# Performance work log

Hardware: AMD Instinct MI355X
Metric: run time of the kernel (lower is better)

Reference implementation:

```python
import jax, jax.numpy as jnp
import numpy as np

TEXT_VOCAB = 32000
CB = 1024          # audio_codebook_size
NCB = 8            # audio_num_codebooks
H = 2048           # hidden_size
NH = 16            # attention heads
NKV = 4            # kv heads (GQA)
HD = H // NH       # head dim = 128
FF = 8192          # ffn intermediate
L = 2              # num layers
EPS = 1e-5


def rmsnorm(x, w):
    v = jnp.mean(x * x, axis=-1, keepdims=True)
    return x * jax.lax.rsqrt(v + EPS) * w


def rope(x, pos):
    # x: [B,S,h,d], rotate-half style RoPE
    d = x.shape[-1]
    inv = 1.0 / (10000.0 ** (jnp.arange(0, d, 2, dtype=jnp.float32) / d))
    ang = pos[:, None] * inv[None, :]                 # [S, d/2]
    cos = jnp.cos(ang)[None, :, None, :]
    sin = jnp.sin(ang)[None, :, None, :]
    x1, x2 = x[..., : d // 2], x[..., d // 2 :]
    return jnp.concatenate([x1 * cos - x2 * sin, x2 * cos + x1 * sin], axis=-1)


def attention(x, wq, wk, wv, wo, pos, mask_bias):
    B, S, _ = x.shape
    q = (x @ wq).reshape(B, S, NH, HD)
    k = (x @ wk).reshape(B, S, NKV, HD)
    v = (x @ wv).reshape(B, S, NKV, HD)
    q = rope(q, pos)
    k = rope(k, pos)
    k = jnp.repeat(k, NH // NKV, axis=2)
    v = jnp.repeat(v, NH // NKV, axis=2)
    scores = jnp.einsum('bqhd,bkhd->bhqk', q, k) / np.float32(np.sqrt(HD))
    p = jax.nn.softmax(scores + mask_bias, axis=-1)
    o = jnp.einsum('bhqk,bkhd->bqhd', p, v).reshape(B, S, NH * HD)
    return o @ wo


def mlp(x, wfc, wproj):
    return jax.nn.silu(x @ wfc) @ wproj


def setup_inputs() -> dict:
    key = jax.random.key(0)
    ks = jax.random.split(key, 20)
    s = 0.02
    inp = {
        'input_ids': jax.random.randint(ks[0], (1, 2048), 0, TEXT_VOCAB + CB, dtype=jnp.int64 if jax.config.jax_enable_x64 else jnp.int32),
        'vocab_emb': jax.random.normal(ks[1], (TEXT_VOCAB, H), jnp.float32) * s,
        'audio_emb': jax.random.normal(ks[2], (NCB * CB, H), jnp.float32) * s,
        'ln_in_text': jnp.ones((L, H), jnp.float32),
        'ln_in_audio': jnp.ones((L, H), jnp.float32),
        'ln_post_text': jnp.ones((L, H), jnp.float32),
        'ln_post_audio': jnp.ones((L, H), jnp.float32),
        'wq': jax.random.normal(ks[3], (L, H, NH * HD), jnp.float32) * s,
        'wk': jax.random.normal(ks[4], (L, H, NKV * HD), jnp.float32) * s,
        'wv': jax.random.normal(ks[5], (L, H, NKV * HD), jnp.float32) * s,
        'wo': jax.random.normal(ks[6], (L, NH * HD, H), jnp.float32) * s,
        'wfc_text': jax.random.normal(ks[7], (L, H, FF), jnp.float32) * s,
        'wproj_text': jax.random.normal(ks[8], (L, FF, H), jnp.float32) * s,
        'wfc_audio': jax.random.normal(ks[9], (L, H, FF), jnp.float32) * s,
        'wproj_audio': jax.random.normal(ks[10], (L, FF, H), jnp.float32) * s,
        'ln_f': jnp.ones((H,), jnp.float32),
    }
    return inp


def reference(input_ids, vocab_emb, audio_emb, ln_in_text, ln_in_audio,
              ln_post_text, ln_post_audio, wq, wk, wv, wo,
              wfc_text, wproj_text, wfc_audio, wproj_audio, ln_f):
    B, S = input_ids.shape
    amask = input_ids > TEXT_VOCAB - 1                      # [B,S] audio-token mask
    text_tok = jnp.where(amask, TEXT_VOCAB - 1, input_ids)
    text_e = vocab_emb[text_tok]                            # [B,S,H]
    audio_tok = jnp.where(amask, input_ids - TEXT_VOCAB, 0)
    shift = (jnp.arange(NCB) * CB)[:, None, None]           # [NCB,1,1]
    audio_e = audio_emb[audio_tok[None] + shift].sum(0)     # sum over codebooks -> [B,S,H]
    h = jnp.where(amask[..., None], audio_e, text_e)

    pos = jnp.arange(S, dtype=jnp.float32)
    causal = jnp.tril(jnp.ones((S, S), bool))
    mask_bias = jnp.where(causal, 0.0, -1e9).astype(jnp.float32)[None, None]
    m = amask[..., None]

    for i in range(L):
        res = h
        hn = jnp.where(m, rmsnorm(h, ln_in_audio[i]), rmsnorm(h, ln_in_text[i]))
        h = res + attention(hn, wq[i], wk[i], wv[i], wo[i], pos, mask_bias)
        res = h
        t = mlp(rmsnorm(h, ln_post_text[i]), wfc_text[i], wproj_text[i])
        a = mlp(rmsnorm(h, ln_post_audio[i]), wfc_audio[i], wproj_audio[i])
        h = res + jnp.where(m, a, t)

    return rmsnorm(h, ln_f)
```

## Files before the change

### kernel.cpp

```cpp
#include <hip/hip_runtime.h>
#include <hip/hip_bf16.h>
#include <math.h>

#define S_LEN 2048
#define HID   2048

typedef __bf16 bf16x8 __attribute__((ext_vector_type(8)));
typedef float  f32x4  __attribute__((ext_vector_type(4)));

__device__ __forceinline__ unsigned short f2b(float x) {
  __hip_bfloat16 h = __float2bfloat16(x);
  return __builtin_bit_cast(unsigned short, h);
}

__device__ __forceinline__ float block_sum_256(float v) {
  __shared__ float red[4];
  #pragma unroll
  for (int o = 32; o > 0; o >>= 1) v += __shfl_down(v, o, 64);
  if ((threadIdx.x & 63) == 0) red[threadIdx.x >> 6] = v;
  __syncthreads();
  v = red[0] + red[1] + red[2] + red[3];
  __syncthreads();
  return v;
}

__device__ __forceinline__ float block_max_256(float v) {
  __shared__ float redm[4];
  #pragma unroll
  for (int o = 32; o > 0; o >>= 1) v = fmaxf(v, __shfl_down(v, o, 64));
  if ((threadIdx.x & 63) == 0) redm[threadIdx.x >> 6] = v;
  __syncthreads();
  v = fmaxf(fmaxf(redm[0], redm[1]), fmaxf(redm[2], redm[3]));
  __syncthreads();
  return v;
}

__global__ __launch_bounds__(256) void embed_kernel(
    const int* __restrict__ ids, const float* __restrict__ vemb,
    const float* __restrict__ aemb, float* __restrict__ h, int* __restrict__ amask) {
  const int s = blockIdx.x;
  const int id = ids[s];
  const bool am = id > 31999;
  if (threadIdx.x == 0) amask[s] = am ? 1 : 0;
  const int d0 = threadIdx.x * 8;
  float out[8];
  if (am) {
    const int at = id - 32000;
    #pragma unroll
    for (int u = 0; u < 8; u++) out[u] = 0.f;
    for (int cb = 0; cb < 8; cb++) {
      const float* src = aemb + (long)(at + cb * 1024) * HID + d0;
      #pragma unroll
      for (int u = 0; u < 8; u++) out[u] += src[u];
    }
  } else {
    const float* src = vemb + (long)id * HID + d0;
    #pragma unroll
    for (int u = 0; u < 8; u++) out[u] = src[u];
  }
  float* dst = h + (long)s * HID + d0;
  #pragma unroll
  for (int u = 0; u < 8; u++) dst[u] = out[u];
}

__global__ __launch_bounds__(256) void partition_rows(
    const int* __restrict__ ids, int* __restrict__ apos, int* __restrict__ cnt) {
  __shared__ int ca[256];
  __shared__ int sc[257];
  const int t = threadIdx.x;
  int m[8], loc = 0;
  #pragma unroll
  for (int i = 0; i < 8; i++) { m[i] = ids[t * 8 + i] > 31999 ? 1 : 0; loc += m[i]; }
  ca[t] = loc;
  __syncthreads();
  if (t == 0) {
    int run = 0;
    for (int i = 0; i < 256; i++) { sc[i] = run; run += ca[i]; }
    sc[256] = run;
  }
  __syncthreads();
  int off = sc[t];
  #pragma unroll
  for (int i = 0; i < 8; i++) {
    const int s = t * 8 + i;
    if (m[i]) { apos[s] = off; off++; }
    else apos[s] = -1;
  }
  if (t == 0) { cnt[0] = sc[256]; cnt[1] = (sc[256] + 127) & ~127; }
}

__global__ __launch_bounds__(256) void transposew(
    const float* __restrict__ W, int ldw, unsigned short* __restrict__ Wt, int K, int N) {
  __shared__ float t[64][65];
  const int k0 = blockIdx.y * 64, n0 = blockIdx.x * 64;
  const int q = threadIdx.x & 15;
  const int r0 = threadIdx.x >> 4;
  #pragma unroll
  for (int i = 0; i < 4; i++) {
    const int row = r0 + i * 16;
    const float4 v = *(const float4*)(W + (long)(k0 + row) * ldw + n0 + q * 4);
    t[row][q * 4 + 0] = v.x; t[row][q * 4 + 1] = v.y;
    t[row][q * 4 + 2] = v.z; t[row][q * 4 + 3] = v.w;
  }
  __syncthreads();
  #pragma unroll
  for (int i = 0; i < 4; i++) {
    const int n = r0 + i * 16;
    ushort4 o;
    o.x = f2b(t[q * 4 + 0][n]); o.y = f2b(t[q * 4 + 1][n]);
    o.z = f2b(t[q * 4 + 2][n]); o.w = f2b(t[q * 4 + 3][n]);
    *(ushort4*)(Wt + (long)(n0 + n) * K + k0 + q * 4) = o;
  }
}

__global__ __launch_bounds__(256) void rope_table(float* __restrict__ c, float* __restrict__ s_) {
  const int i = blockIdx.x * 256 + threadIdx.x;
  const int pos = i >> 6, j = i & 63;
  const float inv = powf(10000.f, -(float)(2 * j) * (1.f / 128.f));
  const float ang = (float)pos * inv;
  c[i] = cosf(ang);
  s_[i] = sinf(ang);
}

__global__ __launch_bounds__(64) void rope_apply(
    const float* __restrict__ qkv, const float* __restrict__ rc, const float* __restrict__ rs,
    unsigned short* __restrict__ qb, unsigned short* __restrict__ kb) {
  const int s = blockIdx.x;
  const int hh = blockIdx.y;
  const int j = threadIdx.x;
  const float c = rc[s * 64 + j], sn = rs[s * 64 + j];
  const float* base;
  unsigned short* out;
  if (hh < 16) {
    base = qkv + (long)s * 3072 + hh * 128;
    out = qb + (long)s * 2048 + hh * 128;
  } else {
    base = qkv + (long)s * 3072 + 2048 + (hh - 16) * 128;
    out = kb + (long)s * 512 + (hh - 16) * 128;
  }
  const float x1 = base[j], x2 = base[j + 64];
  out[j] = f2b(x1 * c - x2 * sn);
  out[j + 64] = f2b(x2 * c + x1 * sn);
}

__global__ __launch_bounds__(256) void rmsnorm_sel(
    const float* __restrict__ x, const int* __restrict__ amask,
    const float* __restrict__ wt, const float* __restrict__ wa, unsigned short* __restrict__ out) {
  const long s = blockIdx.x;
  const float* xr = x + s * HID;
  const int d0 = threadIdx.x * 8;
  float v[8], ss = 0.f;
  #pragma unroll
  for (int u = 0; u < 8; u++) { v[u] = xr[d0 + u]; ss += v[u] * v[u]; }
  ss = block_sum_256(ss) * (1.f / HID);
  const float rr = rsqrtf(ss + 1e-5f);
  const float* w = amask[s] ? wa : wt;
  #pragma unroll
  for (int u = 0; u < 8; u++) out[s * HID + d0 + u] = f2b(v[u] * rr * w[d0 + u]);
}

__global__ __launch_bounds__(256) void rmsnorm_post(
    const float* __restrict__ x, const int* __restrict__ apos,
    const float* __restrict__ wt, const float* __restrict__ wa,
    unsigned short* __restrict__ hnt, unsigned short* __restrict__ hna_g) {
  const long s = blockIdx.x;
  const float* xr = x + s * HID;
  const int d0 = threadIdx.x * 8;
  float v[8], ss = 0.f;
  #pragma unroll
  for (int u = 0; u < 8; u++) { v[u] = xr[d0 + u]; ss += v[u] * v[u]; }
  ss = block_sum_256(ss) * (1.f / HID);
  const float rr = rsqrtf(ss + 1e-5f);
  const int ap = apos[s];
  #pragma unroll
  for (int u = 0; u < 8; u++) {
    const float xn = v[u] * rr;
    hnt[s * HID + d0 + u] = f2b(xn * wt[d0 + u]);
    if (ap >= 0) hna_g[(long)ap * HID + d0 + u] = f2b(xn * wa[d0 + u]);
  }
}

__global__ __launch_bounds__(256) void rmsnorm_final(
    const float* __restrict__ x, const float* __restrict__ w, float* __restrict__ out) {
  const long s = blockIdx.x;
  const float* xr = x + s * HID;
  const int d0 = threadIdx.x * 8;
  float v[8], ss = 0.f;
  #pragma unroll
  for (int u = 0; u < 8; u++) { v[u] = xr[d0 + u]; ss += v[u] * v[u]; }
  ss = block_sum_256(ss) * (1.f / HID);
  const float rr = rsqrtf(ss + 1e-5f);
  #pragma unroll
  for (int u = 0; u < 8; u++) out[s * HID + d0 + u] = v[u] * rr * w[d0 + u];
}

__global__ __launch_bounds__(256) void softmax_rows(
    const float* __restrict__ Sc, unsigned short* __restrict__ P) {
  const long rowg = blockIdx.x;
  const int row = (int)(rowg & (S_LEN - 1));
  const float* x = Sc + rowg * S_LEN;
  unsigned short* p = P + rowg * S_LEN;
  const int d0 = threadIdx.x * 8;
  float v[8], m = -1e30f;
  if (d0 + 7 <= row) {
    #pragma unroll
    for (int u = 0; u < 8; u++) v[u] = x[d0 + u];
  } else if (d0 <= row) {
    #pragma unroll
    for (int u = 0; u < 8; u++) v[u] = (d0 + u <= row) ? x[d0 + u] : -1e30f;
  } else {
    #pragma unroll
    for (int u = 0; u < 8; u++) v[u] = -1e30f;
  }
  #pragma unroll
  for (int u = 0; u < 8; u++) m = fmaxf(m, v[u]);
  m = block_max_256(m);
  float sum = 0.f;
  #pragma unroll
  for (int u = 0; u < 8; u++) { v[u] = expf(v[u] - m); sum += v[u]; }
  sum = block_sum_256(sum);
  const float inv = 1.f / sum;
  if (d0 <= (row | 127)) {
    #pragma unroll
    for (int u = 0; u < 8; u++) p[d0 + u] = f2b(v[u] * inv);
  }
}

__global__ __launch_bounds__(256) void pv_reduce(
    const float* __restrict__ part, unsigned short* __restrict__ o) {
  const int i = blockIdx.x * 256 + threadIdx.x;
  const int z = i >> 18, s = (i >> 7) & 2047, d = i & 127;
  const float v = part[i] + part[i + (1 << 22)] + part[i + 2 * (1 << 22)] + part[i + 3 * (1 << 22)];
  o[(long)s * 2048 + z * 128 + d] = f2b(v);
}

__global__ __launch_bounds__(256) void mlp_reduce(
    const float* __restrict__ pt, const float* __restrict__ pa,
    const int* __restrict__ apos, float* __restrict__ h) {
  const int i = blockIdx.x * 256 + threadIdx.x;
  const int r = i >> 11, c = i & 2047;
  const long Z = (long)1 << 22;
  const int ap = apos[r];
  float val;
  if (ap < 0) {
    val = pt[i] + pt[i + Z] + pt[i + 2 * Z] + pt[i + 3 * Z];
  } else {
    const long b = (long)ap * 2048 + c;
    val = 0.f;
    #pragma unroll
    for (int k = 0; k < 8; k++) val += pa[k * Z + b];
  }
  h[i] += val;
}

__device__ __forceinline__ void gload16(const void* g, void* l) {
  __builtin_amdgcn_global_load_lds((const __attribute__((address_space(1))) void*)g,
                                   (__attribute__((address_space(3))) void*)l, 16, 0, 0);
}

template <int BM, int BN, int EPI>
__global__ __launch_bounds__(512) void gemm2(
    const unsigned short* __restrict__ A, int lda, long sAz,
    const unsigned short* __restrict__ Bt, int ldb, long sBz,
    void* __restrict__ Cv, int ldc, long sCz, long sCx, int K, float scale,
    const int* __restrict__ ecnt, int kspl) {
  constexpr int MF = BM / 32;
  constexpr int NF = BN / 64;
  __shared__ __align__(16) unsigned short smem[2 * (BM + BN) * 64];
  const int tid = threadIdx.x;
  const int lane = tid & 63;
  const int wave = tid >> 6;
  const int bm = blockIdx.y * BM;
  const int z = blockIdx.z;
  int bn, kbeg, nt;
  if constexpr (EPI == 6) {
    bn = 0;
    kbeg = blockIdx.x * 512;
    int keff = bm + BM; if (keff > K) keff = K;
    nt = (keff - kbeg) / 64;
    if (nt < 0) nt = 0;
    if (nt > 8) nt = 8;
  } else if constexpr (EPI == 7) {
    bn = blockIdx.x * BN;
    kbeg = z * kspl;
    nt = kspl / 64;
  } else {
    bn = blockIdx.x * BN;
    kbeg = 0;
    nt = K / 64;
  }
  if constexpr (EPI == 1) {
    if (bn >= bm + BM) return;
  }
  if constexpr (EPI == 2 || EPI == 7) {
    if (bm >= ecnt[1]) return;
  }
  A += sAz * z;
  Bt += sBz * ((EPI == 1 || EPI == 6) ? (z >> 2) : z);
  const int wm = (wave >> 2) * (BM / 2);
  const int wn = (wave & 3) * (BN / 4);
  const int lr = lane & 15;
  const int kg = lane >> 4;
  const int swx = lr & 7;
  const int trow = tid >> 3;
  const int tc = tid & 7;
  const long aoff = (long)(bm + trow) * lda + ((tc ^ (trow & 7)) * 8);
  const long boff = (long)(bn + trow) * ldb + ((tc ^ (trow & 7)) * 8);

  f32x4 acc[MF][NF];
  #pragma unroll
  for (int m = 0; m < MF; m++)
    #pragma unroll
    for (int n = 0; n < NF; n++) acc[m][n] = (f32x4){0.f, 0.f, 0.f, 0.f};

  auto stage = [&](int buf, int k0) {
    unsigned short* sA = &smem[(size_t)buf * (BM + BN) * 64];
    #pragma unroll
    for (int r = 0; r < BM / 64; r++)
      gload16(A + aoff + (long)r * 64 * lda + k0, sA + r * 4096 + tid * 8);
    unsigned short* sB = sA + BM * 64;
    #pragma unroll
    for (int r = 0; r < BN / 64; r++)
      gload16(Bt + boff + (long)r * 64 * ldb + k0, sB + r * 4096 + tid * 8);
  };
  auto compute = [&](int buf) {
    const unsigned short* sA = &smem[(size_t)buf * (BM + BN) * 64];
    const unsigned short* sB = sA + BM * 64;
    #pragma unroll
    for (int ks = 0; ks < 2; ks++) {
      bf16x8 af[MF], bv[NF];
      #pragma unroll
      for (int m = 0; m < MF; m++) {
        const int row = wm + m * 16 + lr;
        af[m] = *(const bf16x8*)(sA + row * 64 + (((ks * 4 + kg) ^ swx) * 8));
      }
      #pragma unroll
      for (int n = 0; n < NF; n++) {
        const int row = wn + n * 16 + lr;
        bv[n] = *(const bf16x8*)(sB + row * 64 + (((ks * 4 + kg) ^ swx) * 8));
      }
      #pragma unroll
      for (int m = 0; m < MF; m++)
        #pragma unroll
        for (int n = 0; n < NF; n++)
          acc[m][n] = __builtin_amdgcn_mfma_f32_16x16x32_bf16(af[m], bv[n], acc[m][n], 0, 0, 0);
    }
  };

  if (nt > 0) {
    stage(0, kbeg);
    asm volatile("s_waitcnt vmcnt(0)" ::: "memory");
    __syncthreads();
    int cur = 0;
    for (int t = 0; t < nt; t++) {
      if (t + 1 < nt) stage(cur ^ 1, kbeg + (t + 1) * 64);
      compute(cur);
      asm volatile("s_waitcnt vmcnt(0)" ::: "memory");
      __syncthreads();
      cur ^= 1;
    }
  }

  #pragma unroll
  for (int m = 0; m < MF; m++) {
    #pragma unroll
    for (int n = 0; n < NF; n++) {
      #pragma unroll
      for (int r = 0; r < 4; r++) {
        const int grow = bm + wm + m * 16 + kg * 4 + r;
        const int gcol = bn + wn + n * 16 + lr;
        const long idx = (long)grow * ldc + gcol;
        float v = acc[m][n][r];
        if constexpr (EPI == 0) {
          ((float*)Cv)[sCz * z + idx] = v;
        } else if constexpr (EPI == 1) {
          v *= scale;
          if (gcol > grow) v = -1e9f;
          ((float*)Cv)[sCz * z + idx] = v;
        } else if constexpr (EPI == 2) {
          ((unsigned short*)Cv)[idx] = f2b(v / (1.f + expf(-v)));
        } else if constexpr (EPI == 3) {
          ((float*)Cv)[idx] += v;
        } else if constexpr (EPI == 6) {
          ((float*)Cv)[(long)blockIdx.x * sCx + sCz * z + idx] = v;
        } else if constexpr (EPI == 7) {
          ((float*)Cv)[(long)z * sCz + idx] = v;
        }
      }
    }
  }
}

template <int EPI>
__global__ __launch_bounds__(512, 1) void gemm8(
    const unsigned short* __restrict__ A0, const unsigned short* __restrict__ A1, int lda,
    const unsigned short* __restrict__ Bt, long sBz, int ldb,
    void* __restrict__ Cv, int ldc, long sCz, int K) {
  __shared__ __align__(16) unsigned short smem[2][4][8192];
  const int tid = threadIdx.x;
  const int lane = tid & 63;
  const int wave = tid >> 6;
  const int bm = blockIdx.y * 256;
  const int bn = blockIdx.x * 256;
  const int z = blockIdx.z;
  const unsigned short* Aq;
  const unsigned short* Bq;
  if constexpr (EPI == 10) {
    Aq = z ? A1 : A0;
    Bq = Bt + (long)z * sBz;
  } else {
    Aq = A0 + z * 2048;
    Bq = Bt + z * 2048;
  }
  const int nt = K / 64;
  const int trow = tid >> 3;
  const int tc = tid & 7;
  const int sws = (tc ^ (trow & 7)) * 8;
  const int lr = lane & 15;
  const int kg = lane >> 4;
  const int wr = (wave >> 2) * 64;
  const int wc = (wave & 3) * 32;

  f32x4 acc[2][2][4][2];
  #pragma unroll
  for (int mh = 0; mh < 2; mh++)
    #pragma unroll
    for (int nh = 0; nh < 2; nh++)
      #pragma unroll
      for (int mf = 0; mf < 4; mf++)
        #pragma unroll
        for (int nf = 0; nf < 2; nf++) acc[mh][nh][mf][nf] = (f32x4){0.f, 0.f, 0.f, 0.f};

  bf16x8 af[2][4], bv0[2][2], bv1[2][2];

  auto stageA = [&](int buf, int half, int k0) {
    const unsigned short* g = Aq + (long)(bm + half * 128 + trow) * lda + k0 + sws;
    unsigned short* l = &smem[buf][half][0] + tid * 8;
    gload16(g, l);
    gload16(g + (long)64 * lda, l + 4096);
  };
  auto stageB = [&](int buf, int half, int k0) {
    const unsigned short* g = Bq + (long)(bn + half * 128 + trow) * ldb + k0 + sws;
    unsigned short* l = &smem[buf][2 + half][0] + tid * 8;
    gload16(g, l);
    gload16(g + (long)64 * ldb, l + 4096);
  };

#define GSYNC(VM) \
  asm volatile("s_waitcnt vmcnt(" #VM ")" ::: "memory"); \
  __builtin_amdgcn_s_barrier(); \
  asm volatile("" ::: "memory"); \
  __builtin_amdgcn_sched_barrier(0)

#define RD_A(BUF, MH) do { \
    _Pragma("unroll") \
    for (int ks = 0; ks < 2; ++ks) { \
      _Pragma("unroll") \
      for (int mf = 0; mf < 4; ++mf) { \
        const int row = wr + mf * 16 + lr; \
        af[ks][mf] = *(const bf16x8*)(&smem[BUF][MH][0] + row * 64 + (((ks * 4 + kg) ^ (row & 7)) * 8)); \
      } \
    } \
  } while (0)

#define RD_B(BUF, NH, BV) do { \
    _Pragma("unroll") \
    for (int ks = 0; ks < 2; ++ks) { \
      _Pragma("unroll") \
      for (int nf = 0; nf < 2; ++nf) { \
        const int row = wc + nf * 16 + lr; \
        BV[ks][nf] = *(const bf16x8*)(&smem[BUF][2 + NH][0] + row * 64 + (((ks * 4 + kg) ^ (row & 7)) * 8)); \
      } \
    } \
  } while (0)

#define DO_MFMA(MH, NH, BV) do { \
    __builtin_amdgcn_s_setprio(1); \
    _Pragma("unroll") \
    for (int ks = 0; ks < 2; ++ks) \
      _Pragma("unroll") \
      for (int mf = 0; mf < 4; ++mf) \
        _Pragma("unroll") \
        for (int nf = 0; nf < 2; ++nf) \
          acc[MH][NH][mf][nf] = __builtin_amdgcn_mfma_f32_16x16x32_bf16( \
              af[ks][mf], BV[ks][nf], acc[MH][NH][mf][nf], 0, 0, 0); \
    __builtin_amdgcn_s_setprio(0); \
  } while (0)

  stageA(0, 0, 0); stageB(0, 0, 0); stageB(0, 1, 0); stageA(0, 1, 0);
  stageA(1, 0, 64); stageB(1, 0, 64); stageB(1, 1, 64);
  GSYNC(10);

  for (int t = 0; t <= nt - 3; ++t) {
    const int b = t & 1, nb = b ^ 1;
    const int k1 = (t + 1) << 6, k2 = (t + 2) << 6;
    RD_A(b, 0); RD_B(b, 0, bv0); stageA(nb, 1, k1); DO_MFMA(0, 0, bv0); GSYNC(10);
    RD_B(b, 1, bv1);             stageA(b, 0, k2);  DO_MFMA(0, 1, bv1); GSYNC(10);
    RD_A(b, 1);                  stageB(b, 0, k2);  DO_MFMA(1, 1, bv1); GSYNC(10);
                                 stageB(b, 1, k2);  DO_MFMA(1, 0, bv0); GSYNC(10);
  }
  {
    const int t = nt - 2;
    const int b = t & 1, nb = b ^ 1;
    const int k1 = (t + 1) << 6;
    RD_A(b, 0); RD_B(b, 0, bv0); stageA(nb, 1, k1); DO_MFMA(0, 0, bv0); GSYNC(10);
    RD_B(b, 1, bv1);                                DO_MFMA(0, 1, bv1); GSYNC(8);
    RD_A(b, 1);                                     DO_MFMA(1, 1, bv1); GSYNC(8);
                                                    DO_MFMA(1, 0, bv0); GSYNC(4);
  }
  {
    const int b = (nt - 1) & 1;
    RD_A(b, 0); RD_B(b, 0, bv0); DO_MFMA(0, 0, bv0); GSYNC(2);
    RD_B(b, 1, bv1);             DO_MFMA(0, 1, bv1); GSYNC(0);
    RD_A(b, 1);                  DO_MFMA(1, 1, bv1); GSYNC(0);
                                 DO_MFMA(1, 0, bv0);
  }
#undef DO_MFMA
#undef RD_B
#undef RD_A
#undef GSYNC

  #pragma unroll
  for (int mh = 0; mh < 2; mh++) {
    #pragma unroll
    for (int nh = 0; nh < 2; nh++) {
      #pragma unroll
      for (int mf = 0; mf < 4; mf++) {
        #pragma unroll
        for (int nf = 0; nf < 2; nf++) {
          #pragma unroll
          for (int r = 0; r < 4; r++) {
            const int grow = bm + mh * 128 + wr + mf * 16 + kg * 4 + r;
            const int gcol = bn + nh * 128 + wc + nf * 16 + lr;
            const long idx = (long)z * sCz + (long)grow * ldc + gcol;
            const float v = acc[mh][nh][mf][nf][r];
            if constexpr (EPI == 10) {
              ((unsigned short*)Cv)[idx] = f2b(v / (1.f + expf(-v)));
            } else {
              ((float*)Cv)[idx] = v;
            }
          }
        }
      }
    }
  }
}

__global__ __launch_bounds__(256) void fill_zero(float* p, long n) {
  const long i = (long)blockIdx.x * 256 + threadIdx.x;
  if (i < n) p[i] = 0.f;
}

extern "C" void kernel_launch(void* const* d_in, const int* in_sizes, int n_in,
                              void* d_out, int out_size, void* d_ws, size_t ws_size,
                              hipStream_t stream) {
  const int* ids = (const int*)d_in[0];
  const float* vocab_emb = (const float*)d_in[1];
  const float* audio_emb = (const float*)d_in[2];
  const float* ln_in_text = (const float*)d_in[3];
  const float* ln_in_audio = (const float*)d_in[4];
  const float* ln_post_text = (const float*)d_in[5];
  const float* ln_post_audio = (const float*)d_in[6];
  const float* wq = (const float*)d_in[7];
  const float* wk = (const float*)d_in[8];
  const float* wv = (const float*)d_in[9];
  const float* wo = (const float*)d_in[10];
  const float* wfc_t = (const float*)d_in[11];
  const float* wpj_t = (const float*)d_in[12];
  const float* wfc_a = (const float*)d_in[13];
  const float* wpj_a = (const float*)d_in[14];
  const float* ln_f = (const float*)d_in[15];

  size_t off = 0;
  auto alloc = [&](size_t bytes) -> void* {
    void* p = (char*)d_ws + off;
    off += (bytes + 255) & ~(size_t)255;
    return p;
  };
  const size_t LW = 77594624;
  unsigned short* wsT = (unsigned short*)alloc((size_t)2 * LW * 2);
  int* amask = (int*)alloc(S_LEN * 4);
  int* apos = (int*)alloc(S_LEN * 4);
  int* cnt = (int*)alloc(16);
  float* ropec = (float*)alloc((size_t)S_LEN * 64 * 4);
  float* ropes = (float*)alloc((size_t)S_LEN * 64 * 4);
  float* h = (float*)alloc((size_t)S_LEN * HID * 4);
  unsigned short* hn = (unsigned short*)alloc((size_t)S_LEN * HID * 2);
  unsigned short* hnt = (unsigned short*)alloc((size_t)S_LEN * HID * 2);
  unsigned short* hna_g = (unsigned short*)alloc((size_t)S_LEN * HID * 2);
  float* qkv = (float*)alloc((size_t)S_LEN * 3072 * 4);
  unsigned short* qb = (unsigned short*)alloc((size_t)S_LEN * 2048 * 2);
  unsigned short* kb = (unsigned short*)alloc((size_t)S_LEN * 512 * 2);
  unsigned short* vt = (unsigned short*)alloc((size_t)512 * S_LEN * 2);
  unsigned short* o = (unsigned short*)alloc((size_t)S_LEN * 2048 * 2);
  char* big = (char*)alloc(402653184);
  float* scores = (float*)big;
  unsigned short* P = (unsigned short*)(big + 268435456);
  float* pv_part = (float*)big;
  unsigned short* mlp_t = (unsigned short*)big;
  unsigned short* mlp_a = (unsigned short*)(big + 33554432);
  float* pt = (float*)(big + 67108864);
  float* pa = (float*)(big + 134217728);

  if (ws_size < off) {
    fill_zero<<<(out_size + 255) / 256, 256, 0, stream>>>((float*)d_out, out_size);
    return;
  }

  const size_t WO_ = 6291456, WFT = 10485760, WPT = 27262976, WFA = 44040192, WPA = 60817408;

  embed_kernel<<<S_LEN, 256, 0, stream>>>(ids, vocab_emb, audio_emb, h, amask);
  partition_rows<<<1, 256, 0, stream>>>(ids, apos, cnt);
  rope_table<<<S_LEN * 64 / 256, 256, 0, stream>>>(ropec, ropes);

  for (int i = 0; i < 2; i++) {
    const size_t wb = (size_t)i * LW;
    transposew<<<dim3(32, 32), 256, 0, stream>>>(wq + (size_t)i * 2048 * 2048, 2048, wsT + wb, 2048, 2048);
    transposew<<<dim3(8, 32), 256, 0, stream>>>(wk + (size_t)i * 2048 * 512, 512, wsT + wb + 4194304, 2048, 512);
    transposew<<<dim3(8, 32), 256, 0, stream>>>(wv + (size_t)i * 2048 * 512, 512, wsT + wb + 5242880, 2048, 512);
    transposew<<<dim3(32, 32), 256, 0, stream>>>(wo + (size_t)i * 2048 * 2048, 2048, wsT + wb + WO_, 2048, 2048);
    transposew<<<dim3(128, 32), 256, 0, stream>>>(wfc_t + (size_t)i * 2048 * 8192, 8192, wsT + wb + WFT, 2048, 8192);
    transposew<<<dim3(32, 128), 256, 0, stream>>>(wpj_t + (size_t)i * 8192 * 2048, 2048, wsT + wb + WPT, 8192, 2048);
    transposew<<<dim3(128, 32), 256, 0, stream>>>(wfc_a + (size_t)i * 2048 * 8192, 8192, wsT + wb + WFA, 2048, 8192);
    transposew<<<dim3(32, 128), 256, 0, stream>>>(wpj_a + (size_t)i * 8192 * 2048, 2048, wsT + wb + WPA, 8192, 2048);
  }

  const float iscale = 0.08838834764831845f;
  for (int i = 0; i < 2; i++) {
    const size_t wb = (size_t)i * LW;
    rmsnorm_sel<<<S_LEN, 256, 0, stream>>>(h, amask, ln_in_text + i * HID, ln_in_audio + i * HID, hn);
    gemm2<128, 128, 0><<<dim3(24, 16, 1), 512, 0, stream>>>(hn, 2048, 0, wsT + wb, 2048, 0,
        qkv, 3072, 0, 0, 2048, 1.f, nullptr, 0);
    rope_apply<<<dim3(S_LEN, 20), 64, 0, stream>>>(qkv, ropec, ropes, qb, kb);
    transposew<<<dim3(8, 32), 256, 0, stream>>>(qkv + 2560, 3072, vt, 2048, 512);
    gemm2<256, 256, 1><<<dim3(8, 8, 16), 512, 0, stream>>>(qb, 2048, 128, kb, 512, 128,
        scores, 2048, (long)S_LEN * S_LEN, 0, 128, iscale, nullptr, 0);
    softmax_rows<<<16 * S_LEN, 256, 0, stream>>>(scores, P);
    gemm2<128, 128, 6><<<dim3(4, 16, 16), 512, 0, stream>>>(P, 2048, (long)S_LEN * S_LEN, vt, 2048, 262144,
        pv_part, 128, 262144, (long)1 << 22, 2048, 1.f, nullptr, 0);
    pv_reduce<<<16384, 256, 0, stream>>>(pv_part, o);
    gemm2<128, 128, 3><<<dim3(16, 16, 1), 512, 0, stream>>>(o, 2048, 0, wsT + wb + WO_, 2048, 0,
        h, 2048, 0, 0, 2048, 1.f, nullptr, 0);
    rmsnorm_post<<<S_LEN, 256, 0, stream>>>(h, apos, ln_post_text + i * HID, ln_post_audio + i * HID, hnt, hna_g);
    gemm2<128, 128, 2><<<dim3(64, 16, 1), 512, 0, stream>>>(hna_g, 2048, 0, wsT + wb + WFA, 2048, 0,
        mlp_a, 8192, 0, 0, 2048, 1.f, cnt, 0);
    gemm8<10><<<dim3(32, 8, 1), 512, 0, stream>>>(hnt, hnt, 2048, wsT + wb + WFT, 0, 2048,
        mlp_t, 8192, 0, 2048);
    gemm2<128, 128, 7><<<dim3(16, 16, 8), 512, 0, stream>>>(mlp_a, 8192, 0, wsT + wb + WPA, 8192, 0,
        pa, 2048, (long)1 << 22, 0, 8192, 1.f, cnt, 1024);
    gemm8<11><<<dim3(8, 8, 4), 512, 0, stream>>>(mlp_t, mlp_t, 8192, wsT + wb + WPT, 0, 8192,
        pt, 2048, (long)1 << 22, 2048);
    mlp_reduce<<<16384, 256, 0, stream>>>(pt, pa, apos, h);
  }
  rmsnorm_final<<<S_LEN, 256, 0, stream>>>(h, ln_f, (float*)d_out);
}
```

Measured before the change: 1.205 ms.

## Replace materialized scores/softmax/PV with fused two-pass flash-style attention

Removes the full 16x2048x2048 fp32 score matrix, the separate softmax kernel and the split-K PV gemm with its reduction. Attention now runs in two fused kernels. The first computes the per-row max and log-sum-exp over causal K tiles. The second recomputes QK^T, forms normalized probabilities in LDS and multiplies by V, splitting the key range into two chunks that a small merge kernel sums. Work is handed out through persistent blocks pulling items from atomic counters, ordered largest-first to balance causal load. This cuts a large amount of HBM traffic, but QK^T is computed twice.

```diff
diff --git a/kernel.cpp b/kernel.cpp
--- a/kernel.cpp
+++ b/kernel.cpp
@@ -20,17 +20,6 @@
   if ((threadIdx.x & 63) == 0) red[threadIdx.x >> 6] = v;
   __syncthreads();
   v = red[0] + red[1] + red[2] + red[3];
-  __syncthreads();
-  return v;
-}
-
-__device__ __forceinline__ float block_max_256(float v) {
-  __shared__ float redm[4];
-  #pragma unroll
-  for (int o = 32; o > 0; o >>= 1) v = fmaxf(v, __shfl_down(v, o, 64));
-  if ((threadIdx.x & 63) == 0) redm[threadIdx.x >> 6] = v;
-  __syncthreads();
-  v = fmaxf(fmaxf(redm[0], redm[1]), fmaxf(redm[2], redm[3]));
   __syncthreads();
   return v;
 }
@@ -88,6 +77,8 @@
   }
   if (t == 0) { cnt[0] = sc[256]; cnt[1] = (sc[256] + 127) & ~127; }
 }
+
+__global__ void init_ctrs(int* c) { c[threadIdx.x] = 0; }
 
 __global__ __launch_bounds__(256) void transposew(
     const float* __restrict__ W, int ldw, unsigned short* __restrict__ Wt, int K, int N) {
@@ -194,44 +185,250 @@
   for (int u = 0; u < 8; u++) out[s * HID + d0 + u] = v[u] * rr * w[d0 + u];
 }
 
-__global__ __launch_bounds__(256) void softmax_rows(
-    const float* __restrict__ Sc, unsigned short* __restrict__ P) {
-  const long rowg = blockIdx.x;
-  const int row = (int)(rowg & (S_LEN - 1));
-  const float* x = Sc + rowg * S_LEN;
-  unsigned short* p = P + rowg * S_LEN;
-  const int d0 = threadIdx.x * 8;
-  float v[8], m = -1e30f;
-  if (d0 + 7 <= row) {
-    #pragma unroll
-    for (int u = 0; u < 8; u++) v[u] = x[d0 + u];
-  } else if (d0 <= row) {
-    #pragma unroll
-    for (int u = 0; u < 8; u++) v[u] = (d0 + u <= row) ? x[d0 + u] : -1e30f;
-  } else {
-    #pragma unroll
-    for (int u = 0; u < 8; u++) v[u] = -1e30f;
-  }
-  #pragma unroll
-  for (int u = 0; u < 8; u++) m = fmaxf(m, v[u]);
-  m = block_max_256(m);
-  float sum = 0.f;
-  #pragma unroll
-  for (int u = 0; u < 8; u++) { v[u] = expf(v[u] - m); sum += v[u]; }
-  sum = block_sum_256(sum);
-  const float inv = 1.f / sum;
-  if (d0 <= (row | 127)) {
-    #pragma unroll
-    for (int u = 0; u < 8; u++) p[d0 + u] = f2b(v[u] * inv);
-  }
-}
-
-__global__ __launch_bounds__(256) void pv_reduce(
-    const float* __restrict__ part, unsigned short* __restrict__ o) {
+__device__ __forceinline__ void gload16(const void* g, void* l) {
+  __builtin_amdgcn_global_load_lds((const __attribute__((address_space(1))) void*)g,
+                                   (__attribute__((address_space(3))) void*)l, 16, 0, 0);
+}
+
+#define ABAR() do { __builtin_amdgcn_s_barrier(); \
+  asm volatile("" ::: "memory"); __builtin_amdgcn_sched_barrier(0); } while (0)
+
+__global__ __launch_bounds__(256) void attn_pass1(
+    const unsigned short* __restrict__ qb, const unsigned short* __restrict__ kb,
+    float* __restrict__ mstat, int* __restrict__ ctr, float iscale) {
+  __shared__ __align__(16) unsigned short Kb[2][2][128][64];
+  __shared__ int s_item;
+  const int tid = threadIdx.x;
+  const int lane = tid & 63;
+  const int w = tid >> 6;
+  const int lr = lane & 15;
+  const int kg = lane >> 4;
+  const int trow = tid >> 3;
+  const int tc = tid & 7;
+
+  for (;;) {
+    if (tid == 0) s_item = atomicAdd(ctr, 1);
+    __syncthreads();
+    const int item = s_item;
+    __syncthreads();
+    if (item >= 512) break;
+    const int q64 = 31 - (item >> 4);
+    const int h = item & 15;
+    const int kvh = h >> 2;
+    const int bm = q64 * 64;
+    const int nt = (bm >> 7) + 1;
+
+    bf16x8 af_q[4];
+    {
+      const unsigned short* qr = qb + (long)(bm + w * 16 + lr) * 2048 + h * 128 + kg * 8;
+      #pragma unroll
+      for (int c = 0; c < 4; c++) af_q[c] = *(const bf16x8*)(qr + c * 32);
+    }
+    float m[4], l[4];
+    #pragma unroll
+    for (int r = 0; r < 4; r++) { m[r] = -1e30f; l[r] = 0.f; }
+
+    auto stageK = [&](int buf, int t) {
+      const int kv0 = t * 128;
+      #pragma unroll
+      for (int hh2 = 0; hh2 < 2; hh2++)
+        #pragma unroll
+        for (int rr = 0; rr < 4; rr++) {
+          const int row = trow + rr * 32;
+          gload16(kb + (long)(kv0 + row) * 512 + kvh * 128 + hh2 * 64 + ((tc ^ (row & 7)) * 8),
+                  &Kb[buf][hh2][row][tc * 8]);
+        }
+    };
+
+    stageK(0, 0);
+    for (int t = 0; t < nt; t++) {
+      const bool hn = (t + 1) < nt;
+      if (hn) stageK((t + 1) & 1, t + 1);
+      if (hn) { asm volatile("s_waitcnt vmcnt(8)" ::: "memory"); }
+      else    { asm volatile("s_waitcnt vmcnt(0)" ::: "memory"); }
+      ABAR();
+      f32x4 acc[8];
+      #pragma unroll
+      for (int nf = 0; nf < 8; nf++) acc[nf] = (f32x4){0.f, 0.f, 0.f, 0.f};
+      #pragma unroll
+      for (int c = 0; c < 4; c++) {
+        #pragma unroll
+        for (int nf = 0; nf < 8; nf++) {
+          const int row = nf * 16 + lr;
+          bf16x8 bk = *(const bf16x8*)(&Kb[t & 1][c >> 1][row][(((c & 1) * 4 + kg) ^ (row & 7)) * 8]);
+          acc[nf] = __builtin_amdgcn_mfma_f32_16x16x32_bf16(af_q[c], bk, acc[nf], 0, 0, 0);
+        }
+      }
+      const bool diag = !hn;
+      #pragma unroll
+      for (int r = 0; r < 4; r++) {
+        const int rowg = bm + w * 16 + kg * 4 + r;
+        float sv[8], tmax = -1e30f;
+        #pragma unroll
+        for (int nf = 0; nf < 8; nf++) {
+          float s = acc[nf][r] * iscale;
+          const int colg = t * 128 + nf * 16 + lr;
+          if (diag && colg > rowg) s = -1e30f;
+          sv[nf] = s;
+          tmax = fmaxf(tmax, s);
+        }
+        #pragma unroll
+        for (int o = 1; o < 16; o <<= 1) tmax = fmaxf(tmax, __shfl_xor(tmax, o, 64));
+        const float mn = fmaxf(m[r], tmax);
+        float psum = 0.f;
+        #pragma unroll
+        for (int nf = 0; nf < 8; nf++) psum += __expf(sv[nf] - mn);
+        #pragma unroll
+        for (int o = 1; o < 16; o <<= 1) psum += __shfl_xor(psum, o, 64);
+        l[r] = l[r] * __expf(m[r] - mn) + psum;
+        m[r] = mn;
+      }
+      ABAR();
+    }
+    if (lr == 0) {
+      #pragma unroll
+      for (int r = 0; r < 4; r++)
+        mstat[h * 2048 + bm + w * 16 + kg * 4 + r] = m[r] + __logf(l[r]);
+    }
+    __syncthreads();
+  }
+}
+
+__global__ __launch_bounds__(512, 1) void attn_pass2(
+    const unsigned short* __restrict__ qb, const unsigned short* __restrict__ kb,
+    const unsigned short* __restrict__ vt, const float* __restrict__ mstat,
+    float* __restrict__ opart, int* __restrict__ ctr, float iscale) {
+  __shared__ __align__(16) unsigned short Kb[2][2][128][64];
+  __shared__ __align__(16) unsigned short Vb[2][128][64];
+  __shared__ __align__(16) unsigned short Pb[8][16][144];
+  __shared__ int s_item;
+  const int tid = threadIdx.x;
+  const int lane = tid & 63;
+  const int w = tid >> 6;
+  const int lr = lane & 15;
+  const int kg = lane >> 4;
+  const int trow = tid >> 3;
+  const int tc = tid & 7;
+
+  for (;;) {
+    if (tid == 0) s_item = atomicAdd(ctr, 1);
+    __syncthreads();
+    const int item = s_item;
+    __syncthreads();
+    if (item >= 512) break;
+    const int qq = 15 - (item >> 5);
+    const int h = item & 15;
+    const int cch = (item >> 4) & 1;
+    const int kvh = h >> 2;
+    const int bm = qq * 128;
+    const int nt = qq + 1;
+    const int tmid = (nt + 1) >> 1;
+    const int t0 = cch ? tmid : 0;
+    const int t1 = cch ? nt : tmid;
+    if (t0 >= t1) continue;
+
+    bf16x8 af_q[4];
+    {
+      const unsigned short* qr = qb + (long)(bm + w * 16 + lr) * 2048 + h * 128 + kg * 8;
+      #pragma unroll
+      for (int c = 0; c < 4; c++) af_q[c] = *(const bf16x8*)(qr + c * 32);
+    }
+    float mm_r[4];
+    #pragma unroll
+    for (int r = 0; r < 4; r++) mm_r[r] = mstat[h * 2048 + bm + w * 16 + kg * 4 + r];
+    f32x4 acc_o[8];
+    #pragma unroll
+    for (int nf = 0; nf < 8; nf++) acc_o[nf] = (f32x4){0.f, 0.f, 0.f, 0.f};
+
+    auto stageK = [&](int buf, int t) {
+      const int kv0 = t * 128;
+      #pragma unroll
+      for (int hh2 = 0; hh2 < 2; hh2++)
+        #pragma unroll
+        for (int rr = 0; rr < 2; rr++) {
+          const int row = trow + rr * 64;
+          gload16(kb + (long)(kv0 + row) * 512 + kvh * 128 + hh2 * 64 + ((tc ^ (row & 7)) * 8),
+                  &Kb[buf][hh2][row][tc * 8]);
+        }
+    };
+    auto stageV = [&](int t) {
+      const int kv0 = t * 128;
+      #pragma unroll
+      for (int hh2 = 0; hh2 < 2; hh2++)
+        #pragma unroll
+        for (int rr = 0; rr < 2; rr++) {
+          const int row = trow + rr * 64;
+          gload16(vt + (long)(kvh * 128 + row) * 2048 + kv0 + hh2 * 64 + ((tc ^ (row & 7)) * 8),
+                  &Vb[hh2][row][tc * 8]);
+        }
+    };
+
+    stageK(t0 & 1, t0);
+    for (int t = t0; t < t1; t++) {
+      const bool hn = (t + 1) < t1;
+      stageV(t);
+      if (hn) stageK((t + 1) & 1, t + 1);
+      if (hn) { asm volatile("s_waitcnt vmcnt(8)" ::: "memory"); }
+      else    { asm volatile("s_waitcnt vmcnt(4)" ::: "memory"); }
+      ABAR();
+      f32x4 acc[8];
+      #pragma unroll
+      for (int nf = 0; nf < 8; nf++) acc[nf] = (f32x4){0.f, 0.f, 0.f, 0.f};
+      #pragma unroll
+      for (int c = 0; c < 4; c++) {
+        #pragma unroll
+        for (int nf = 0; nf < 8; nf++) {
+          const int row = nf * 16 + lr;
+          bf16x8 bk = *(const bf16x8*)(&Kb[t & 1][c >> 1][row][(((c & 1) * 4 + kg) ^ (row & 7)) * 8]);
+          acc[nf] = __builtin_amdgcn_mfma_f32_16x16x32_bf16(af_q[c], bk, acc[nf], 0, 0, 0);
+        }
+      }
+      const bool diag = (t == nt - 1);
+      #pragma unroll
+      for (int nf = 0; nf < 8; nf++) {
+        #pragma unroll
+        for (int r = 0; r < 4; r++) {
+          float s = acc[nf][r] * iscale;
+          const int colg = t * 128 + nf * 16 + lr;
+          const int rowg = bm + w * 16 + kg * 4 + r;
+          if (diag && colg > rowg) s = -1e30f;
+          Pb[w][kg * 4 + r][nf * 16 + lr] = f2b(__expf(s - mm_r[r]));
+        }
+      }
+      asm volatile("s_waitcnt lgkmcnt(0)" ::: "memory");
+      __builtin_amdgcn_sched_barrier(0);
+      if (hn) { asm volatile("s_waitcnt vmcnt(4)" ::: "memory"); }
+      else    { asm volatile("s_waitcnt vmcnt(0)" ::: "memory"); }
+      ABAR();
+      #pragma unroll
+      for (int c = 0; c < 4; c++) {
+        bf16x8 ap = *(const bf16x8*)(&Pb[w][lr][c * 32 + kg * 8]);
+        #pragma unroll
+        for (int nf = 0; nf < 8; nf++) {
+          const int row = nf * 16 + lr;
+          bf16x8 bv = *(const bf16x8*)(&Vb[c >> 1][row][(((c & 1) * 4 + kg) ^ (row & 7)) * 8]);
+          acc_o[nf] = __builtin_amdgcn_mfma_f32_16x16x32_bf16(ap, bv, acc_o[nf], 0, 0, 0);
+        }
+      }
+      ABAR();
+    }
+    float* op = opart + (long)cch * 4194304;
+    #pragma unroll
+    for (int nf = 0; nf < 8; nf++)
+      #pragma unroll
+      for (int r = 0; r < 4; r++)
+        op[(long)(bm + w * 16 + kg * 4 + r) * 2048 + h * 128 + nf * 16 + lr] = acc_o[nf][r];
+    __syncthreads();
+  }
+}
+
+__global__ __launch_bounds__(256) void o_merge(
+    const float* __restrict__ op, unsigned short* __restrict__ o) {
   const int i = blockIdx.x * 256 + threadIdx.x;
-  const int z = i >> 18, s = (i >> 7) & 2047, d = i & 127;
-  const float v = part[i] + part[i + (1 << 22)] + part[i + 2 * (1 << 22)] + part[i + 3 * (1 << 22)];
-  o[(long)s * 2048 + z * 128 + d] = f2b(v);
+  const int row = i >> 11;
+  float v = op[i];
+  if (row >= 128) v += op[4194304 + i];
+  o[i] = f2b(v);
 }
 
 __global__ __launch_bounds__(256) void mlp_reduce(
@@ -251,11 +448,6 @@
     for (int k = 0; k < 8; k++) val += pa[k * Z + b];
   }
   h[i] += val;
-}
-
-__device__ __forceinline__ void gload16(const void* g, void* l) {
-  __builtin_amdgcn_global_load_lds((const __attribute__((address_space(1))) void*)g,
-                                   (__attribute__((address_space(3))) void*)l, 16, 0, 0);
 }
 
 template <int BM, int BN, int EPI>
@@ -273,14 +465,7 @@
   const int bm = blockIdx.y * BM;
   const int z = blockIdx.z;
   int bn, kbeg, nt;
-  if constexpr (EPI == 6) {
-    bn = 0;
-    kbeg = blockIdx.x * 512;
-    int keff = bm + BM; if (keff > K) keff = K;
-    nt = (keff - kbeg) / 64;
-    if (nt < 0) nt = 0;
-    if (nt > 8) nt = 8;
-  } else if constexpr (EPI == 7) {
+  if constexpr (EPI == 7) {
     bn = blockIdx.x * BN;
     kbeg = z * kspl;
     nt = kspl / 64;
@@ -289,14 +474,11 @@
     kbeg = 0;
     nt = K / 64;
   }
-  if constexpr (EPI == 1) {
-    if (bn >= bm + BM) return;
-  }
   if constexpr (EPI == 2 || EPI == 7) {
     if (bm >= ecnt[1]) return;
   }
   A += sAz * z;
-  Bt += sBz * ((EPI == 1 || EPI == 6) ? (z >> 2) : z);
+  Bt += sBz * z;
   const int wm = (wave >> 2) * (BM / 2);
   const int wn = (wave & 3) * (BN / 4);
   const int lr = lane & 15;
@@ -373,16 +555,10 @@
         float v = acc[m][n][r];
         if constexpr (EPI == 0) {
           ((float*)Cv)[sCz * z + idx] = v;
-        } else if constexpr (EPI == 1) {
-          v *= scale;
-          if (gcol > grow) v = -1e9f;
-          ((float*)Cv)[sCz * z + idx] = v;
         } else if constexpr (EPI == 2) {
           ((unsigned short*)Cv)[idx] = f2b(v / (1.f + expf(-v)));
         } else if constexpr (EPI == 3) {
           ((float*)Cv)[idx] += v;
-        } else if constexpr (EPI == 6) {
-          ((float*)Cv)[(long)blockIdx.x * sCx + sCz * z + idx] = v;
         } else if constexpr (EPI == 7) {
           ((float*)Cv)[(long)z * sCz + idx] = v;
         }
@@ -582,6 +758,7 @@
   int* amask = (int*)alloc(S_LEN * 4);
   int* apos = (int*)alloc(S_LEN * 4);
   int* cnt = (int*)alloc(16);
+  int* ctrs = (int*)alloc(16);
   float* ropec = (float*)alloc((size_t)S_LEN * 64 * 4);
   float* ropes = (float*)alloc((size_t)S_LEN * 64 * 4);
   float* h = (float*)alloc((size_t)S_LEN * HID * 4);
@@ -593,10 +770,9 @@
   unsigned short* kb = (unsigned short*)alloc((size_t)S_LEN * 512 * 2);
   unsigned short* vt = (unsigned short*)alloc((size_t)512 * S_LEN * 2);
   unsigned short* o = (unsigned short*)alloc((size_t)S_LEN * 2048 * 2);
-  char* big = (char*)alloc(402653184);
-  float* scores = (float*)big;
-  unsigned short* P = (unsigned short*)(big + 268435456);
-  float* pv_part = (float*)big;
+  float* mstat = (float*)alloc((size_t)16 * 2048 * 4);
+  char* big = (char*)alloc(268435456);
+  float* opart = (float*)big;
   unsigned short* mlp_t = (unsigned short*)big;
   unsigned short* mlp_a = (unsigned short*)(big + 33554432);
   float* pt = (float*)(big + 67108864);
@@ -611,6 +787,7 @@
 
   embed_kernel<<<S_LEN, 256, 0, stream>>>(ids, vocab_emb, audio_emb, h, amask);
   partition_rows<<<1, 256, 0, stream>>>(ids, apos, cnt);
+  init_ctrs<<<1, 4, 0, stream>>>(ctrs);
   rope_table<<<S_LEN * 64 / 256, 256, 0, stream>>>(ropec, ropes);
 
   for (int i = 0; i < 2; i++) {
@@ -633,12 +810,9 @@
         qkv, 3072, 0, 0, 2048, 1.f, nullptr, 0);
     rope_apply<<<dim3(S_LEN, 20), 64, 0, stream>>>(qkv, ropec, ropes, qb, kb);
     transposew<<<dim3(8, 32), 256, 0, stream>>>(qkv + 2560, 3072, vt, 2048, 512);
-    gemm2<256, 256, 1><<<dim3(8, 8, 16), 512, 0, stream>>>(qb, 2048, 128, kb, 512, 128,
-        scores, 2048, (long)S_LEN * S_LEN, 0, 128, iscale, nullptr, 0);
-    softmax_rows<<<16 * S_LEN, 256, 0, stream>>>(scores, P);
-    gemm2<128, 128, 6><<<dim3(4, 16, 16), 512, 0, stream>>>(P, 2048, (long)S_LEN * S_LEN, vt, 2048, 262144,
-        pv_part, 128, 262144, (long)1 << 22, 2048, 1.f, nullptr, 0);
-    pv_reduce<<<16384, 256, 0, stream>>>(pv_part, o);
+    attn_pass1<<<256, 256, 0, stream>>>(qb, kb, mstat, ctrs + i * 2, iscale);
+    attn_pass2<<<256, 512, 0, stream>>>(qb, kb, vt, mstat, opart, ctrs + i * 2 + 1, iscale);
+    o_merge<<<16384, 256, 0, stream>>>(opart, o);
     gemm2<128, 128, 3><<<dim3(16, 16, 1), 512, 0, stream>>>(o, 2048, 0, wsT + wb + WO_, 2048, 0,
         h, 2048, 0, 0, 2048, 1.f, nullptr, 0);
     rmsnorm_post<<<S_LEN, 256, 0, stream>>>(h, apos, ln_post_text + i * HID, ln_post_audio + i * HID, hnt, hna_g);
```

After: 1.070 ms. 1.13x faster.
